# Performance work log

Measured on AMD Instinct MI355X. Metric: run time of the kernel, lower is better.

## Reference

```python
import jax, jax.numpy as jnp
import numpy as np

D = 64       # desc_dim
PD = 64      # pose_dim
NH = 4       # num_heads
PS = 5       # patch_size
B, N, H, W = 16, 1024, 256, 256


def setup_inputs() -> dict:
    key = jax.random.key(0)
    ks = jax.random.split(key, 16)
    s = 1.0 / np.sqrt(D)
    inp = {
        "desc_points": jax.random.normal(ks[0], (B, N, D), jnp.float32),
        "shared_feat_map": jax.random.normal(ks[1], (B, D, H, W), jnp.float32),
        "coords": jax.random.randint(ks[2], (B, N, 2), 0, H),
        "pose_embed": jax.random.normal(ks[3], (B, PD), jnp.float32),
        "Wq": jax.random.normal(ks[4], (D, D), jnp.float32) * s,
        "bq": jnp.zeros((D,), jnp.float32),
        "Wk": jax.random.normal(ks[5], (D, D), jnp.float32) * s,
        "bk": jnp.zeros((D,), jnp.float32),
        "Wv": jax.random.normal(ks[6], (D, D), jnp.float32) * s,
        "bv": jnp.zeros((D,), jnp.float32),
        "Wp": jax.random.normal(ks[7], (PD, D), jnp.float32) * s,
        "bp": jnp.zeros((D,), jnp.float32),
        "Wo": jax.random.normal(ks[8], (D, D), jnp.float32) * s,
        "bo": jnp.zeros((D,), jnp.float32),
    }
    return inp


def _patch_means(feat_map, coords):
    # feat_map: [B,C,H,W], coords: [B,N,2] int (y,x). Vectorized ROI mean-pool.
    pad = PS // 2
    padded = jnp.pad(feat_map, ((0, 0), (0, 0), (pad, pad), (pad, pad)))
    y = coords[..., 0]
    x = coords[..., 1]
    off = jnp.arange(PS)
    rows = y[:, :, None, None] + off[None, None, :, None]   # [B,N,PS,1]
    cols = x[:, :, None, None] + off[None, None, None, :]   # [B,N,1,PS]
    bidx = jnp.arange(feat_map.shape[0])[:, None, None, None]
    # advanced indexing: result [B,N,PS,PS,C]
    patches = padded[bidx, :, rows, cols]
    return patches.mean(axis=(2, 3))  # [B,N,C]


def reference(desc_points, shared_feat_map, coords, pose_embed,
              Wq, bq, Wk, bk, Wv, bv, Wp, bp, Wo, bo):
    b, n, c = desc_points.shape
    hd = c // NH
    patch_feats = _patch_means(shared_feat_map, coords)  # [B,N,C]

    q = (desc_points @ Wq + bq).reshape(b, n, NH, hd)
    k = (patch_feats @ Wk + bk).reshape(b, n, NH, hd)
    v = (patch_feats @ Wv + bv).reshape(b, n, NH, hd)

    scores = jnp.einsum('bnhd,bmhd->bhnm', q, k) / jnp.sqrt(jnp.float32(hd))
    probs = jax.nn.softmax(scores, axis=-1)
    attn = jnp.einsum('bhnm,bmhd->bnhd', probs, v).reshape(b, n, c)

    pose_mod = pose_embed @ Wp + bp               # [B,C]
    fused = attn * (1.0 + pose_mod[:, None, :])   # [B,N,C]
    return fused @ Wo + bo
```

## Files before the change

kernel.cpp:

```cpp
#include <hip/hip_runtime.h>
#include <cstdint>
#include <cstddef>

#define BB 16
#define NN 1024
#define DD 64
#define NHH 4
#define HDD 16
#define CAP 64

#define OFF_Q   0
#define OFF_K   (OFF_Q + BB*NHH*NN*HDD)
#define OFF_V   (OFF_K + BB*NHH*NN*HDD)
#define OFF_PM  (OFF_V + BB*NHH*NN*HDD)
#define OFF_AP  (OFF_PM + 1024)
#define OFF_CNT (OFF_AP + BB*NN*DD)
#define OFF_LST (OFF_CNT + BB*256)
#define OFF_PP  (OFF_LST + BB*256*CAP)
#define NEED_FULL ((size_t)(OFF_PP + (size_t)BB*NN*5*DD) * 4)

#define SL 260

__global__ __launch_bounds__(256) void k_zero_cnt(int* __restrict__ cnt)
{
    int t = threadIdx.x;
    int4 z = make_int4(0, 0, 0, 0);
    int4* c4 = (int4*)cnt;
    #pragma unroll
    for (int j = 0; j < 4; ++j) c4[t * 4 + j] = z;
}

__global__ __launch_bounds__(256) void k_bin(
    const int* __restrict__ coords, int* __restrict__ cnt, int* __restrict__ lst)
{
    int pid = blockIdx.x * 256 + threadIdx.x;
    int y = coords[pid * 2 + 0];
    int x = coords[pid * 2 + 1];
    int b = pid >> 10;
    int slot = atomicAdd(&cnt[b * 256 + y], 1);
    if (slot < CAP) lst[(b * 256 + y) * CAP + slot] = (pid << 8) | x;
}

__global__ __launch_bounds__(256) void k_thsum_part(
    const float* __restrict__ fm,
    const int* __restrict__ cnt, const int* __restrict__ lst,
    float* __restrict__ pp)
{
    __shared__ float L[32 * SL];
    int t   = threadIdx.x;
    int bid = blockIdx.x;
    int b   = bid >> 9;
    int y   = (bid >> 1) & 255;
    int ch  = bid & 1;

    int w = t >> 6, l = t & 63;
    const float* src = fm + ((size_t)b << 22) + ((size_t)(ch * 32) << 16) + ((size_t)y << 8);
    #pragma unroll
    for (int i = 0; i < 8; ++i) {
        int c = w * 8 + i;
        float4 v = *(const float4*)(src + ((size_t)c << 16) + l * 4);
        float pz = __shfl_up(v.z, 1);
        float pw = __shfl_up(v.w, 1);
        float nx = __shfl_down(v.x, 1);
        float ny = __shfl_down(v.y, 1);
        if (l == 0)  { pz = 0.f; pw = 0.f; }
        if (l == 63) { nx = 0.f; ny = 0.f; }
        float s3 = v.x + v.y + v.z;
        float s4 = s3 + v.w;
        float4 hs;
        hs.x = pz + pw + s3;
        hs.y = pw + s4;
        hs.z = s4 + nx;
        hs.w = v.y + v.z + v.w + nx + ny;
        *(float4*)(&L[c * SL + 4 * l]) = hs;
    }
    __syncthreads();

    int c  = t & 31;
    int ps = t >> 5;
    #pragma unroll
    for (int dy = -2; dy <= 2; ++dy) {
        int yy = y + dy;
        if ((unsigned)yy < 256u) {
            int base = b * 256 + yy;
            int nc = cnt[base];
            if (nc > CAP) nc = CAP;
            int slot = 2 - dy;
            for (int s0 = ps; s0 < nc; s0 += 8) {
                int e   = lst[base * CAP + s0];
                int pid = e >> 8;
                int x   = e & 255;
                pp[(size_t)pid * 320 + slot * 64 + ch * 32 + c] = L[c * SL + x];
            }
        }
    }
}

__global__ __launch_bounds__(256) void k_pf_qkv_part(
    const float* __restrict__ desc, const float* __restrict__ pp,
    const int* __restrict__ coords,
    const float* __restrict__ Wq, const float* __restrict__ bq,
    const float* __restrict__ Wk, const float* __restrict__ bk,
    const float* __restrict__ Wv, const float* __restrict__ bv,
    float* __restrict__ Q, float* __restrict__ K, float* __restrict__ V)
{
    int w   = threadIdx.x >> 6;
    int c   = threadIdx.x & 63;
    int pid = blockIdx.x * 4 + w;
    int b   = pid >> 10;
    int n   = pid & 1023;

    __shared__ float spf[4][64];
    __shared__ float sd[4][64];

    int y = coords[pid * 2 + 0];
    const float* pprow = pp + (size_t)pid * 320 + c;
    float s = 0.f;
    #pragma unroll
    for (int j = 0; j < 5; ++j) {
        int yy = y + j - 2;
        if ((unsigned)yy < 256u) s += pprow[j * 64];
    }
    spf[w][c] = s * 0.04f;
    sd[w][c]  = desc[(size_t)pid * 64 + c];
    __syncthreads();

    float aq = bq[c], ak = bk[c], av = bv[c];
    #pragma unroll 8
    for (int i = 0; i < 64; ++i) {
        float xd = sd[w][i];
        float xp = spf[w][i];
        aq = fmaf(xd, Wq[i * 64 + c], aq);
        ak = fmaf(xp, Wk[i * 64 + c], ak);
        av = fmaf(xp, Wv[i * 64 + c], av);
    }
    int h = c >> 4, d = c & 15;
    size_t o = (((size_t)b * 4 + h) * 1024 + n) * 16 + d;
    Q[o] = aq; K[o] = ak; V[o] = av;
}

__global__ __launch_bounds__(256) void k_pf_qkv(
    const float* __restrict__ desc, const float* __restrict__ fm,
    const int* __restrict__ coords,
    const float* __restrict__ Wq, const float* __restrict__ bq,
    const float* __restrict__ Wk, const float* __restrict__ bk,
    const float* __restrict__ Wv, const float* __restrict__ bv,
    float* __restrict__ Q, float* __restrict__ K, float* __restrict__ V)
{
    int w   = threadIdx.x >> 6;
    int c   = threadIdx.x & 63;
    int pid = blockIdx.x * 4 + w;
    int b   = pid >> 10;
    int n   = pid & 1023;

    __shared__ float spf[4][64];
    __shared__ float sd[4][64];

    int y = coords[pid * 2 + 0];
    int x = coords[pid * 2 + 1];

    const float* fmc = fm + ((size_t)(b * 64 + c) << 16);
    float s = 0.f;
    #pragma unroll
    for (int dy = -2; dy <= 2; ++dy) {
        int yy = y + dy;
        if ((unsigned)yy < 256u) {
            const float* row = fmc + yy * 256;
            #pragma unroll
            for (int dx = -2; dx <= 2; ++dx) {
                int xx = x + dx;
                if ((unsigned)xx < 256u) s += row[xx];
            }
        }
    }
    spf[w][c] = s * 0.04f;
    sd[w][c]  = desc[(size_t)pid * 64 + c];
    __syncthreads();

    float aq = bq[c], ak = bk[c], av = bv[c];
    #pragma unroll 8
    for (int i = 0; i < 64; ++i) {
        float xd = sd[w][i];
        float xp = spf[w][i];
        aq = fmaf(xd, Wq[i * 64 + c], aq);
        ak = fmaf(xp, Wk[i * 64 + c], ak);
        av = fmaf(xp, Wv[i * 64 + c], av);
    }
    int h = c >> 4, d = c & 15;
    size_t o = (((size_t)b * 4 + h) * 1024 + n) * 16 + d;
    Q[o] = aq; K[o] = ak; V[o] = av;
}

__global__ __launch_bounds__(64) void k_pose(
    const float* __restrict__ pe, const float* __restrict__ Wp,
    const float* __restrict__ bp, float* __restrict__ pm1)
{
    int b = blockIdx.x, c = threadIdx.x;
    __shared__ float sp[64];
    sp[c] = pe[b * 64 + c];
    __syncthreads();
    float acc = bp[c];
    #pragma unroll 8
    for (int i = 0; i < 64; ++i) acc = fmaf(sp[i], Wp[i * 64 + c], acc);
    pm1[b * 64 + c] = 1.f + acc;
}

__global__ __launch_bounds__(256, 2) void k_attn4(
    const float* __restrict__ Q, const float* __restrict__ K,
    const float* __restrict__ V, const float* __restrict__ pm1,
    float* __restrict__ AP)
{
    int bh = blockIdx.x;
    int qc = blockIdx.y;
    int b  = bh >> 2, h = bh & 3;
    int t  = threadIdx.x;
    int ql = t & 31;
    int ks = t >> 5;

    float4 q[4][4];
    float4 A[4][4];
    float  l[4];
    const float4* qp = (const float4*)Q + ((size_t)bh * 1024 + qc * 128 + ql * 4) * 4;
    #pragma unroll
    for (int i = 0; i < 4; ++i) {
        #pragma unroll
        for (int j = 0; j < 4; ++j) { q[i][j] = qp[i * 4 + j]; A[i][j] = make_float4(0.f,0.f,0.f,0.f); }
        l[i] = 0.f;
    }

    const float4* Kb = (const float4*)K + ((size_t)bh * 1024 + ks * 128) * 4;
    const float4* Vb = (const float4*)V + ((size_t)bh * 1024 + ks * 128) * 4;

    for (int m = 0; m < 128; ++m) {
        float4 ka = Kb[m*4+0], kb = Kb[m*4+1], kc = Kb[m*4+2], kd = Kb[m*4+3];
        float4 va = Vb[m*4+0], vb = Vb[m*4+1], vc = Vb[m*4+2], vd = Vb[m*4+3];
        #pragma unroll
        for (int i = 0; i < 4; ++i) {
            float sc = q[i][0].x*ka.x + q[i][0].y*ka.y + q[i][0].z*ka.z + q[i][0].w*ka.w
                     + q[i][1].x*kb.x + q[i][1].y*kb.y + q[i][1].z*kb.z + q[i][1].w*kb.w
                     + q[i][2].x*kc.x + q[i][2].y*kc.y + q[i][2].z*kc.z + q[i][2].w*kc.w
                     + q[i][3].x*kd.x + q[i][3].y*kd.y + q[i][3].z*kd.z + q[i][3].w*kd.w;
            float p = __expf(sc * 0.25f);
            l[i] += p;
            A[i][0].x = fmaf(p, va.x, A[i][0].x); A[i][0].y = fmaf(p, va.y, A[i][0].y);
            A[i][0].z = fmaf(p, va.z, A[i][0].z); A[i][0].w = fmaf(p, va.w, A[i][0].w);
            A[i][1].x = fmaf(p, vb.x, A[i][1].x); A[i][1].y = fmaf(p, vb.y, A[i][1].y);
            A[i][1].z = fmaf(p, vb.z, A[i][1].z); A[i][1].w = fmaf(p, vb.w, A[i][1].w);
            A[i][2].x = fmaf(p, vc.x, A[i][2].x); A[i][2].y = fmaf(p, vc.y, A[i][2].y);
            A[i][2].z = fmaf(p, vc.z, A[i][2].z); A[i][2].w = fmaf(p, vc.w, A[i][2].w);
            A[i][3].x = fmaf(p, vd.x, A[i][3].x); A[i][3].y = fmaf(p, vd.y, A[i][3].y);
            A[i][3].z = fmaf(p, vd.z, A[i][3].z); A[i][3].w = fmaf(p, vd.w, A[i][3].w);
        }
    }

    #pragma unroll
    for (int i = 0; i < 4; ++i) {
        #pragma unroll
        for (int j = 0; j < 4; ++j) {
            A[i][j].x += __shfl_xor(A[i][j].x, 32);
            A[i][j].y += __shfl_xor(A[i][j].y, 32);
            A[i][j].z += __shfl_xor(A[i][j].z, 32);
            A[i][j].w += __shfl_xor(A[i][j].w, 32);
        }
        l[i] += __shfl_xor(l[i], 32);
    }

    __shared__ float sA[4][32][4][16];
    __shared__ float sL[4][32][4];
    int wv = t >> 6, lane = t & 63;
    if (lane < 32) {
        #pragma unroll
        for (int i = 0; i < 4; ++i) {
            float4* dst = (float4*)&sA[wv][ql][i][0];
            dst[0] = A[i][0]; dst[1] = A[i][1]; dst[2] = A[i][2]; dst[3] = A[i][3];
            sL[wv][ql][i] = l[i];
        }
    }
    __syncthreads();

    if (t < 128) {
        int qlr = t >> 2, qir = t & 3;
        float4 o0 = make_float4(0.f,0.f,0.f,0.f), o1 = o0, o2 = o0, o3 = o0;
        float lt = 0.f;
        #pragma unroll
        for (int w2 = 0; w2 < 4; ++w2) {
            const float4* sp4 = (const float4*)&sA[w2][qlr][qir][0];
            float4 a0 = sp4[0], a1 = sp4[1], a2 = sp4[2], a3 = sp4[3];
            o0.x += a0.x; o0.y += a0.y; o0.z += a0.z; o0.w += a0.w;
            o1.x += a1.x; o1.y += a1.y; o1.z += a1.z; o1.w += a1.w;
            o2.x += a2.x; o2.y += a2.y; o2.z += a2.z; o2.w += a2.w;
            o3.x += a3.x; o3.y += a3.y; o3.z += a3.z; o3.w += a3.w;
            lt += sL[w2][qlr][qir];
        }
        float inv = 1.f / lt;
        const float4* pm = (const float4*)(pm1 + b * 64 + h * 16);
        float4 p0 = pm[0], p1 = pm[1], p2 = pm[2], p3 = pm[3];
        float* op = AP + ((size_t)b * 1024 + qc * 128 + t) * 64 + h * 16;
        float4 o;
        o.x = o0.x*inv*p0.x; o.y = o0.y*inv*p0.y; o.z = o0.z*inv*p0.z; o.w = o0.w*inv*p0.w;
        *(float4*)(op + 0) = o;
        o.x = o1.x*inv*p1.x; o.y = o1.y*inv*p1.y; o.z = o1.z*inv*p1.z; o.w = o1.w*inv*p1.w;
        *(float4*)(op + 4) = o;
        o.x = o2.x*inv*p2.x; o.y = o2.y*inv*p2.y; o.z = o2.z*inv*p2.z; o.w = o2.w*inv*p2.w;
        *(float4*)(op + 8) = o;
        o.x = o3.x*inv*p3.x; o.y = o3.y*inv*p3.y; o.z = o3.z*inv*p3.z; o.w = o3.w*inv*p3.w;
        *(float4*)(op + 12) = o;
    }
}

__global__ __launch_bounds__(256) void k_out2(
    const float* __restrict__ AP, const float* __restrict__ Wo,
    const float* __restrict__ bo, float* __restrict__ out)
{
    int w   = threadIdx.x >> 6;
    int c   = threadIdx.x & 63;
    int pid = blockIdx.x * 4 + w;

    __shared__ float sf[4][64];
    sf[w][c] = AP[(size_t)pid * 64 + c];
    __syncthreads();

    float acc = bo[c];
    #pragma unroll 8
    for (int i = 0; i < 64; ++i) acc = fmaf(sf[w][i], Wo[i * 64 + c], acc);
    out[(size_t)pid * 64 + c] = acc;
}

extern "C" void kernel_launch(void* const* d_in, const int* in_sizes, int n_in,
                              void* d_out, int out_size, void* d_ws, size_t ws_size,
                              hipStream_t stream)
{
    const float* desc = (const float*)d_in[0];
    const float* fm   = (const float*)d_in[1];
    const int*   crd  = (const int*)  d_in[2];
    const float* pe   = (const float*)d_in[3];
    const float* Wq   = (const float*)d_in[4];
    const float* bq   = (const float*)d_in[5];
    const float* Wk   = (const float*)d_in[6];
    const float* bk   = (const float*)d_in[7];
    const float* Wv   = (const float*)d_in[8];
    const float* bv   = (const float*)d_in[9];
    const float* Wp   = (const float*)d_in[10];
    const float* bp   = (const float*)d_in[11];
    const float* Wo   = (const float*)d_in[12];
    const float* bo   = (const float*)d_in[13];
    float* out = (float*)d_out;

    float* ws  = (float*)d_ws;
    float* Qb  = ws + OFF_Q;
    float* Kb  = ws + OFF_K;
    float* Vb  = ws + OFF_V;
    float* pm1 = ws + OFF_PM;
    float* AP  = ws + OFF_AP;
    int*   cnt = (int*)(ws + OFF_CNT);
    int*   lst = (int*)(ws + OFF_LST);
    float* pp  = ws + OFF_PP;

    if (ws_size >= NEED_FULL) {
        hipLaunchKernelGGL(k_zero_cnt, dim3(1), dim3(256), 0, stream, cnt);
        hipLaunchKernelGGL(k_bin, dim3(BB * NN / 256), dim3(256), 0, stream, crd, cnt, lst);
        hipLaunchKernelGGL(k_thsum_part, dim3(BB * 256 * 2), dim3(256), 0, stream,
                           fm, cnt, lst, pp);
        hipLaunchKernelGGL(k_pf_qkv_part, dim3(BB * NN / 4), dim3(256), 0, stream,
                           desc, pp, crd, Wq, bq, Wk, bk, Wv, bv, Qb, Kb, Vb);
    } else {
        hipLaunchKernelGGL(k_pf_qkv, dim3(BB * NN / 4), dim3(256), 0, stream,
                           desc, fm, crd, Wq, bq, Wk, bk, Wv, bv, Qb, Kb, Vb);
    }
    hipLaunchKernelGGL(k_pose, dim3(BB), dim3(64), 0, stream, pe, Wp, bp, pm1);
    hipLaunchKernelGGL(k_attn4, dim3(64, 8), dim3(256), 0, stream,
                       Qb, Kb, Vb, pm1, AP);
    hipLaunchKernelGGL(k_out2, dim3(BB * NN / 4), dim3(256), 0, stream,
                       AP, Wo, bo, out);
}
```

Baseline: 529.5 us.

## Stage K/V tiles in shared memory for attention and prescale Q

The attention kernel now loads K and V cooperatively in 256-key tiles into LDS, where all key-split groups read them, instead of each thread streaming its own key range from global memory. The LDS buffer is reused for the final cross-wave reduction, and the 0.25 score scale is folded into Q at load time. This adds block-wide barriers per tile and more LDS traffic in exchange for coalesced global loads and fewer global reads.

```diff
diff --git a/kernel.cpp b/kernel.cpp
--- a/kernel.cpp
+++ b/kernel.cpp
@@ -205,7 +205,7 @@
     pm1[b * 64 + c] = 1.f + acc;
 }
 
-__global__ __launch_bounds__(256, 2) void k_attn4(
+__global__ __launch_bounds__(256, 2) void k_attn6(
     const float* __restrict__ Q, const float* __restrict__ K,
     const float* __restrict__ V, const float* __restrict__ pm1,
     float* __restrict__ AP)
@@ -217,6 +217,10 @@
     int ql = t & 31;
     int ks = t >> 5;
 
+    __shared__ float smem[8704];
+    float* sK = smem;
+    float* sV = smem + 4096;
+
     float4 q[4][4];
     float4 A[4][4];
     float  l[4];
@@ -224,32 +228,57 @@
     #pragma unroll
     for (int i = 0; i < 4; ++i) {
         #pragma unroll
-        for (int j = 0; j < 4; ++j) { q[i][j] = qp[i * 4 + j]; A[i][j] = make_float4(0.f,0.f,0.f,0.f); }
+        for (int j = 0; j < 4; ++j) {
+            float4 v = qp[i * 4 + j];
+            v.x *= 0.25f; v.y *= 0.25f; v.z *= 0.25f; v.w *= 0.25f;
+            q[i][j] = v;
+            A[i][j] = make_float4(0.f, 0.f, 0.f, 0.f);
+        }
         l[i] = 0.f;
     }
 
-    const float4* Kb = (const float4*)K + ((size_t)bh * 1024 + ks * 128) * 4;
-    const float4* Vb = (const float4*)V + ((size_t)bh * 1024 + ks * 128) * 4;
-
-    for (int m = 0; m < 128; ++m) {
-        float4 ka = Kb[m*4+0], kb = Kb[m*4+1], kc = Kb[m*4+2], kd = Kb[m*4+3];
-        float4 va = Vb[m*4+0], vb = Vb[m*4+1], vc = Vb[m*4+2], vd = Vb[m*4+3];
+    const float4* Kg = (const float4*)K + ((size_t)bh << 12);
+    const float4* Vg = (const float4*)V + ((size_t)bh << 12);
+
+    for (int T = 0; T < 4; ++T) {
+        if (T) __syncthreads();
         #pragma unroll
-        for (int i = 0; i < 4; ++i) {
-            float sc = q[i][0].x*ka.x + q[i][0].y*ka.y + q[i][0].z*ka.z + q[i][0].w*ka.w
-                     + q[i][1].x*kb.x + q[i][1].y*kb.y + q[i][1].z*kb.z + q[i][1].w*kb.w
-                     + q[i][2].x*kc.x + q[i][2].y*kc.y + q[i][2].z*kc.z + q[i][2].w*kc.w
-                     + q[i][3].x*kd.x + q[i][3].y*kd.y + q[i][3].z*kd.z + q[i][3].w*kd.w;
-            float p = __expf(sc * 0.25f);
-            l[i] += p;
-            A[i][0].x = fmaf(p, va.x, A[i][0].x); A[i][0].y = fmaf(p, va.y, A[i][0].y);
-            A[i][0].z = fmaf(p, va.z, A[i][0].z); A[i][0].w = fmaf(p, va.w, A[i][0].w);
-            A[i][1].x = fmaf(p, vb.x, A[i][1].x); A[i][1].y = fmaf(p, vb.y, A[i][1].y);
-            A[i][1].z = fmaf(p, vb.z, A[i][1].z); A[i][1].w = fmaf(p, vb.w, A[i][1].w);
-            A[i][2].x = fmaf(p, vc.x, A[i][2].x); A[i][2].y = fmaf(p, vc.y, A[i][2].y);
-            A[i][2].z = fmaf(p, vc.z, A[i][2].z); A[i][2].w = fmaf(p, vc.w, A[i][2].w);
-            A[i][3].x = fmaf(p, vd.x, A[i][3].x); A[i][3].y = fmaf(p, vd.y, A[i][3].y);
-            A[i][3].z = fmaf(p, vd.z, A[i][3].z); A[i][3].w = fmaf(p, vd.w, A[i][3].w);
+        for (int p = 0; p < 4; ++p) {
+            int f = p * 256 + t;
+            ((float4*)sK)[f] = Kg[T * 1024 + f];
+            ((float4*)sV)[f] = Vg[T * 1024 + f];
+        }
+        __syncthreads();
+
+        const float* kb0 = sK + (ks * 32) * 16;
+        const float* vb0 = sV + (ks * 32) * 16;
+        #pragma unroll 2
+        for (int mm = 0; mm < 32; ++mm) {
+            float4 ka = *(const float4*)(kb0 + mm * 16 + 0);
+            float4 kb = *(const float4*)(kb0 + mm * 16 + 4);
+            float4 kc = *(const float4*)(kb0 + mm * 16 + 8);
+            float4 kd = *(const float4*)(kb0 + mm * 16 + 12);
+            float4 va = *(const float4*)(vb0 + mm * 16 + 0);
+            float4 vb = *(const float4*)(vb0 + mm * 16 + 4);
+            float4 vc = *(const float4*)(vb0 + mm * 16 + 8);
+            float4 vd = *(const float4*)(vb0 + mm * 16 + 12);
+            #pragma unroll
+            for (int i = 0; i < 4; ++i) {
+                float sc = q[i][0].x*ka.x + q[i][0].y*ka.y + q[i][0].z*ka.z + q[i][0].w*ka.w
+                         + q[i][1].x*kb.x + q[i][1].y*kb.y + q[i][1].z*kb.z + q[i][1].w*kb.w
+                         + q[i][2].x*kc.x + q[i][2].y*kc.y + q[i][2].z*kc.z + q[i][2].w*kc.w
+                         + q[i][3].x*kd.x + q[i][3].y*kd.y + q[i][3].z*kd.z + q[i][3].w*kd.w;
+                float p = __expf(sc);
+                l[i] += p;
+                A[i][0].x = fmaf(p, va.x, A[i][0].x); A[i][0].y = fmaf(p, va.y, A[i][0].y);
+                A[i][0].z = fmaf(p, va.z, A[i][0].z); A[i][0].w = fmaf(p, va.w, A[i][0].w);
+                A[i][1].x = fmaf(p, vb.x, A[i][1].x); A[i][1].y = fmaf(p, vb.y, A[i][1].y);
+                A[i][1].z = fmaf(p, vb.z, A[i][1].z); A[i][1].w = fmaf(p, vb.w, A[i][1].w);
+                A[i][2].x = fmaf(p, vc.x, A[i][2].x); A[i][2].y = fmaf(p, vc.y, A[i][2].y);
+                A[i][2].z = fmaf(p, vc.z, A[i][2].z); A[i][2].w = fmaf(p, vc.w, A[i][2].w);
+                A[i][3].x = fmaf(p, vd.x, A[i][3].x); A[i][3].y = fmaf(p, vd.y, A[i][3].y);
+                A[i][3].z = fmaf(p, vd.z, A[i][3].z); A[i][3].w = fmaf(p, vd.w, A[i][3].w);
+            }
         }
     }
 
@@ -265,15 +294,16 @@
         l[i] += __shfl_xor(l[i], 32);
     }
 
-    __shared__ float sA[4][32][4][16];
-    __shared__ float sL[4][32][4];
+    __syncthreads();
+    float* sAf = smem;
+    float* sLf = smem + 8192;
     int wv = t >> 6, lane = t & 63;
     if (lane < 32) {
         #pragma unroll
         for (int i = 0; i < 4; ++i) {
-            float4* dst = (float4*)&sA[wv][ql][i][0];
+            float4* dst = (float4*)(sAf + ((wv * 32 + ql) * 4 + i) * 16);
             dst[0] = A[i][0]; dst[1] = A[i][1]; dst[2] = A[i][2]; dst[3] = A[i][3];
-            sL[wv][ql][i] = l[i];
+            sLf[(wv * 32 + ql) * 4 + i] = l[i];
         }
     }
     __syncthreads();
@@ -284,13 +314,13 @@
         float lt = 0.f;
         #pragma unroll
         for (int w2 = 0; w2 < 4; ++w2) {
-            const float4* sp4 = (const float4*)&sA[w2][qlr][qir][0];
+            const float4* sp4 = (const float4*)(sAf + ((w2 * 32 + qlr) * 4 + qir) * 16);
             float4 a0 = sp4[0], a1 = sp4[1], a2 = sp4[2], a3 = sp4[3];
             o0.x += a0.x; o0.y += a0.y; o0.z += a0.z; o0.w += a0.w;
             o1.x += a1.x; o1.y += a1.y; o1.z += a1.z; o1.w += a1.w;
             o2.x += a2.x; o2.y += a2.y; o2.z += a2.z; o2.w += a2.w;
             o3.x += a3.x; o3.y += a3.y; o3.z += a3.z; o3.w += a3.w;
-            lt += sL[w2][qlr][qir];
+            lt += sLf[(w2 * 32 + qlr) * 4 + qir];
         }
         float inv = 1.f / lt;
         const float4* pm = (const float4*)(pm1 + b * 64 + h * 16);
@@ -368,7 +398,7 @@
                            desc, fm, crd, Wq, bq, Wk, bk, Wv, bv, Qb, Kb, Vb);
     }
     hipLaunchKernelGGL(k_pose, dim3(BB), dim3(64), 0, stream, pe, Wp, bp, pm1);
-    hipLaunchKernelGGL(k_attn4, dim3(64, 8), dim3(256), 0, stream,
+    hipLaunchKernelGGL(k_attn6, dim3(64, 8), dim3(256), 0, stream,
                        Qb, Kb, Vb, pm1, AP);
     hipLaunchKernelGGL(k_out2, dim3(BB * NN / 4), dim3(256), 0, stream,
                        AP, Wo, bo, out);
```

After: 530.0 us. Within noise of the previous version (+0.1%).
